# Performance work log

Hardware: AMD Instinct MI355X
Metric: run time of the kernel (lower is better)

Reference implementation:

```python
import jax, jax.numpy as jnp
import numpy as np

EPS = 1e-6
DIM = 384; HEADS = 6; POINTS = 4; LEVELS = 3; HIDDEN = 96
B = 2; H0 = 48; W0 = 48

def layernorm(x, w, b):
    m = jnp.mean(x, -1, keepdims=True)
    v = jnp.var(x, -1, keepdims=True)
    return (x - m) * jax.lax.rsqrt(v + EPS) * w + b

def make_ref_points(shapes):
    # normalized (x, y) pixel centers concatenated over levels -> [N, 2]
    pts = []
    for (Hl, Wl) in shapes:
        ry = (jnp.arange(Hl, dtype=jnp.float32) + 0.5) / Hl
        rx = (jnp.arange(Wl, dtype=jnp.float32) + 0.5) / Wl
        gy, gx = jnp.meshgrid(ry, rx, indexing='ij')
        pts.append(jnp.stack([gx.ravel(), gy.ravel()], -1))
    return jnp.concatenate(pts, 0)

def bilinear_gather(v, x, y, Hl, Wl):
    # v: [B, heads, Hl*Wl, c]; x, y: [B, heads, M] pixel coords
    # matches torch grid_sample(bilinear, align_corners=False, padding zeros)
    x0f = jnp.floor(x); y0f = jnp.floor(y)
    wx = (x - x0f)[..., None]; wy = (y - y0f)[..., None]
    x0 = x0f.astype(jnp.int32); y0 = y0f.astype(jnp.int32)
    def tap(yy, xx):
        valid = ((yy >= 0) & (yy < Hl) & (xx >= 0) & (xx < Wl)).astype(v.dtype)
        idx = jnp.clip(yy, 0, Hl - 1) * Wl + jnp.clip(xx, 0, Wl - 1)
        return jnp.take_along_axis(v, idx[..., None], axis=2) * valid[..., None]
    return (tap(y0, x0) * (1 - wx) * (1 - wy) + tap(y0, x0 + 1) * wx * (1 - wy)
            + tap(y0 + 1, x0) * (1 - wx) * wy + tap(y0 + 1, x0 + 1) * wx * wy)

def msdeform_attn(q, f, shapes, Wv, bv, Woff, boff, Watt, batt, Wout, bout):
    Bq, Nq, C = q.shape
    c = C // HEADS
    value = (f @ Wv + bv).reshape(Bq, -1, HEADS, c)
    off = (q @ Woff + boff).reshape(Bq, Nq, HEADS, LEVELS, POINTS, 2)
    att = jax.nn.softmax((q @ Watt + batt).reshape(Bq, Nq, HEADS, LEVELS * POINTS), -1)
    att = att.reshape(Bq, Nq, HEADS, LEVELS, POINTS)
    ref = make_ref_points(shapes)  # [Nq, 2]
    norm = jnp.array([[wl, hl] for (hl, wl) in shapes], dtype=q.dtype)  # [L, 2] = (W, H)
    loc = ref[None, :, None, None, None, :] + off / norm[None, None, None, :, None, :]
    starts = np.cumsum([0] + [h * w for (h, w) in shapes])
    out = jnp.zeros((Bq, Nq, HEADS, c), q.dtype)
    for l, (Hl, Wl) in enumerate(shapes):
        vl = value[:, starts[l]:starts[l + 1]].transpose(0, 2, 1, 3)  # [B,h,HW,c]
        ll = loc[:, :, :, l]  # [B,N,h,P,2]
        x = (ll[..., 0] * Wl - 0.5).transpose(0, 2, 1, 3).reshape(Bq, HEADS, Nq * POINTS)
        y = (ll[..., 1] * Hl - 0.5).transpose(0, 2, 1, 3).reshape(Bq, HEADS, Nq * POINTS)
        s = bilinear_gather(vl, x, y, Hl, Wl).reshape(Bq, HEADS, Nq, POINTS, c)
        out = out + jnp.einsum('bhnpc,bnhp->bnhc', s, att[:, :, :, l])
    return out.reshape(Bq, Nq, C) @ Wout + bout

def dwconv_levels(x, shapes, dw_w, dw_b):
    Bq, N, C = x.shape
    outs, s = [], 0
    for (Hl, Wl) in shapes:
        xi = x[:, s:s + Hl * Wl].reshape(Bq, Hl, Wl, C)
        yi = jax.lax.conv_general_dilated(xi, dw_w, (1, 1), 'SAME',
             dimension_numbers=('NHWC', 'HWIO', 'NHWC'), feature_group_count=C) + dw_b
        outs.append(yi.reshape(Bq, Hl * Wl, C))
        s += Hl * Wl
    return jnp.concatenate(outs, 1)

def setup_inputs():
    key = jax.random.key(0)
    ks = jax.random.split(key, 16)
    n = (H0 * W0) // 4
    N = 21 * n
    wfn = lambda k, s: 0.02 * jax.random.normal(k, s, jnp.float32)
    ones = lambda s: jnp.ones(s, jnp.float32)
    zeros = lambda s: jnp.zeros(s, jnp.float32)
    return {
        'query': jax.random.normal(ks[0], (B, N, DIM), jnp.float32),
        'reference_points': jax.random.uniform(ks[1], (B, N, 1, 2), dtype=jnp.float32),
        'feat': jax.random.normal(ks[2], (B, 4 * n, DIM), jnp.float32),
        'spatial_shapes': jnp.array([[2 * H0, 2 * W0], [H0, W0], [H0 // 2, W0 // 2]], jnp.int32),
        'level_start_index': jnp.array([0, 16 * n, 20 * n], jnp.int32),
        'H': H0, 'W': W0,
        'cti_qnorm_w': ones((DIM,)), 'cti_qnorm_b': zeros((DIM,)),
        'cti_fnorm_w': ones((DIM,)), 'cti_fnorm_b': zeros((DIM,)),
        'cf_qnorm_w': ones((DIM,)), 'cf_qnorm_b': zeros((DIM,)),
        'cf_fnorm_w': ones((DIM,)), 'cf_fnorm_b': zeros((DIM,)),
        'Wv': wfn(ks[3], (DIM, DIM)), 'bv': zeros((DIM,)),
        'Woff': wfn(ks[4], (DIM, HEADS * LEVELS * POINTS * 2)), 'boff': zeros((HEADS * LEVELS * POINTS * 2,)),
        'Watt': wfn(ks[5], (DIM, HEADS * LEVELS * POINTS)), 'batt': zeros((HEADS * LEVELS * POINTS,)),
        'Wout': wfn(ks[6], (DIM, DIM)), 'bout': zeros((DIM,)),
        'ffn_norm_w': ones((DIM,)), 'ffn_norm_b': zeros((DIM,)),
        'fc1_w': wfn(ks[7], (DIM, HIDDEN)), 'fc1_b': zeros((HIDDEN,)),
        'dw_w': wfn(ks[8], (3, 3, 1, HIDDEN)), 'dw_b': zeros((HIDDEN,)),
        'fc2_w': wfn(ks[9], (HIDDEN, DIM)), 'fc2_b': zeros((DIM,)),
    }

def reference(query, reference_points, feat, spatial_shapes, level_start_index, H, W,
              cti_qnorm_w, cti_qnorm_b, cti_fnorm_w, cti_fnorm_b,
              cf_qnorm_w, cf_qnorm_b, cf_fnorm_w, cf_fnorm_b,
              Wv, bv, Woff, boff, Watt, batt, Wout, bout,
              ffn_norm_w, ffn_norm_b, fc1_w, fc1_b, dw_w, dw_b, fc2_w, fc2_b):
    # NOTE: passed reference_points/spatial_shapes/level_start_index are ignored by
    # CTI_toC.forward; it recomputes them via deform_inputs_only_one(query, 16H, 16W).
    Bq, N, C = query.shape
    n = N // 21
    q = jnp.concatenate([query[:, :16 * n], query[:, 16 * n:20 * n] + feat, query[:, 20 * n:]], 1)
    shapes = [(2 * H, 2 * W), (H, W), (H // 2, W // 2)]
    qn = layernorm(q, cti_qnorm_w, cti_qnorm_b)
    fn = layernorm(q, cti_fnorm_w, cti_fnorm_b)
    aq = layernorm(qn, cf_qnorm_w, cf_qnorm_b)
    af = layernorm(fn, cf_fnorm_w, cf_fnorm_b)
    attn = msdeform_attn(aq, af, shapes, Wv, bv, Woff, boff, Watt, batt, Wout, bout)
    out = qn + attn
    h = layernorm(out, ffn_norm_w, ffn_norm_b) @ fc1_w + fc1_b
    h = dwconv_levels(h, shapes, dw_w, dw_b)
    h = jax.nn.gelu(h, approximate=False)
    h = h @ fc2_w + fc2_b
    return out + h
```

## Files before the change

### kernel.cpp

```cpp
#include <hip/hip_runtime.h>
#include <hip/hip_bf16.h>
#include <hip/hip_fp16.h>
#include <cstdint>
#include <cstddef>

#define NB 2
#define NTOK 12096
#define TOKS (NB * NTOK)
#define DIMC 384
#define NHEADS 6
#define CHD 64

typedef __attribute__((ext_vector_type(8))) __bf16 bf16x8;
typedef __attribute__((ext_vector_type(4))) float f32x4;

__device__ __forceinline__ float wave_reduce_add(float v) {
#pragma unroll
  for (int o = 32; o > 0; o >>= 1) v += __shfl_xor(v, o, 64);
  return v;
}

__device__ __forceinline__ float bf_lo(uint u) {
  union { uint i; float f; } c; c.i = u << 16; return c.f;
}
__device__ __forceinline__ float bf_hi(uint u) {
  union { uint i; float f; } c; c.i = u & 0xffff0000u; return c.f;
}
__device__ __forceinline__ ushort f2bf(float x) {
  union { __hip_bfloat16 b; ushort u; } c; c.b = __float2bfloat16(x); return c.u;
}

__device__ __forceinline__ void gload16(const ushort* g, ushort* l) {
  __builtin_amdgcn_global_load_lds(
      (const __attribute__((address_space(1))) uint*)g,
      (__attribute__((address_space(3))) uint*)l, 16, 0, 0);
}

__global__ __launch_bounds__(256) void prelude_kernel(
    const float* __restrict__ Wv, const float* __restrict__ Woff,
    const float* __restrict__ Watt, const float* __restrict__ Wo,
    const float* __restrict__ fc1, const float* __restrict__ fc2,
    const float* __restrict__ boff, const float* __restrict__ batt,
    const float* __restrict__ fc1b,
    __hip_bfloat16* __restrict__ Wvt, __hip_bfloat16* __restrict__ Wot,
    __hip_bfloat16* __restrict__ Wofat, __hip_bfloat16* __restrict__ fc1t,
    __hip_bfloat16* __restrict__ fc2t, float* __restrict__ bofat,
    float* __restrict__ fc1bp,
    const float* __restrict__ query, const float* __restrict__ feat,
    const float* __restrict__ w1, const float* __restrict__ b1,
    const float* __restrict__ w2, const float* __restrict__ b2,
    const float* __restrict__ w3, const float* __restrict__ b3,
    const float* __restrict__ w4, const float* __restrict__ b4,
    __hip_bfloat16* __restrict__ qn, __hip_bfloat16* __restrict__ aq,
    __hip_bfloat16* __restrict__ af) {
  if (blockIdx.x < 576) {
    int id = blockIdx.x * 256 + threadIdx.x;
    int k = id % 384, n = id / 384;
    Wvt[(size_t)n * 384 + k] = __float2bfloat16(Wv[(size_t)k * 384 + n]);
    Wot[(size_t)n * 384 + k] = __float2bfloat16(Wo[(size_t)k * 384 + n]);
    if (n < 256) {
      float v = 0.f;
      if (n < 144) v = Woff[(size_t)k * 144 + n];
      else if (n < 216) v = Watt[(size_t)k * 72 + (n - 144)];
      Wofat[(size_t)n * 384 + k] = __float2bfloat16(v);
    }
    if (n < 128)
      fc1t[(size_t)n * 384 + k] = __float2bfloat16(n < 96 ? fc1[(size_t)k * 96 + n] : 0.f);
    if (k < 96)
      fc2t[(size_t)n * 96 + k] = __float2bfloat16(fc2[(size_t)k * 384 + n]);
    if (id < 256) bofat[id] = id < 144 ? boff[id] : (id < 216 ? batt[id - 144] : 0.f);
    if (id < 128) fc1bp[id] = id < 96 ? fc1b[id] : 0.f;
    return;
  }

  int wid = ((blockIdx.x - 576) * blockDim.x + threadIdx.x) >> 6;
  if (wid >= TOKS) return;
  int lane = threadIdx.x & 63;
  int bb = wid / NTOK;
  int nq = wid - bb * NTOK;

  float x[6];
  const float* qp = query + (size_t)wid * DIMC + lane;
#pragma unroll
  for (int i = 0; i < 6; ++i) x[i] = qp[64 * i];
  if (nq >= 9216 && nq < 11520) {
    const float* fp = feat + ((size_t)bb * 2304 + (nq - 9216)) * DIMC + lane;
#pragma unroll
    for (int i = 0; i < 6; ++i) x[i] += fp[64 * i];
  }

  float s = 0.f, ss = 0.f;
#pragma unroll
  for (int i = 0; i < 6; ++i) { s += x[i]; ss += x[i] * x[i]; }
  s = wave_reduce_add(s); ss = wave_reduce_add(ss);
  float mean = s * (1.f / DIMC);
  float rs = rsqrtf(ss * (1.f / DIMC) - mean * mean + 1e-6f);

  float qv[6], fv[6];
  __hip_bfloat16* qnp = qn + (size_t)wid * DIMC + lane;
#pragma unroll
  for (int i = 0; i < 6; ++i) {
    int e = lane + 64 * i;
    float xh = (x[i] - mean) * rs;
    qv[i] = xh * w1[e] + b1[e];
    fv[i] = xh * w2[e] + b2[e];
    qnp[64 * i] = __float2bfloat16(qv[i]);
  }

  s = 0.f; ss = 0.f;
#pragma unroll
  for (int i = 0; i < 6; ++i) { s += qv[i]; ss += qv[i] * qv[i]; }
  s = wave_reduce_add(s); ss = wave_reduce_add(ss);
  float m2 = s * (1.f / DIMC);
  float rs2 = rsqrtf(ss * (1.f / DIMC) - m2 * m2 + 1e-6f);
  __hip_bfloat16* aqp = aq + (size_t)wid * DIMC + lane;
#pragma unroll
  for (int i = 0; i < 6; ++i) {
    int e = lane + 64 * i;
    aqp[64 * i] = __float2bfloat16((qv[i] - m2) * rs2 * w3[e] + b3[e]);
  }

  s = 0.f; ss = 0.f;
#pragma unroll
  for (int i = 0; i < 6; ++i) { s += fv[i]; ss += fv[i] * fv[i]; }
  s = wave_reduce_add(s); ss = wave_reduce_add(ss);
  float m3 = s * (1.f / DIMC);
  float rs3 = rsqrtf(ss * (1.f / DIMC) - m3 * m3 + 1e-6f);
  __hip_bfloat16* afp = af + (size_t)wid * DIMC + lane;
#pragma unroll
  for (int i = 0; i < 6; ++i) {
    int e = lane + 64 * i;
    afp[64 * i] = __float2bfloat16((fv[i] - m3) * rs3 * w4[e] + b4[e]);
  }
}

__global__ __launch_bounds__(256) void ln_kernel(
    const float* __restrict__ x, const float* __restrict__ w,
    const float* __restrict__ b, __hip_bfloat16* __restrict__ y) {
  int wid = (blockIdx.x * blockDim.x + threadIdx.x) >> 6;
  if (wid >= TOKS) return;
  int lane = threadIdx.x & 63;
  float v[6];
  const float* xp = x + (size_t)wid * DIMC + lane;
#pragma unroll
  for (int i = 0; i < 6; ++i) v[i] = xp[64 * i];
  float s = 0.f, ss = 0.f;
#pragma unroll
  for (int i = 0; i < 6; ++i) { s += v[i]; ss += v[i] * v[i]; }
  s = wave_reduce_add(s); ss = wave_reduce_add(ss);
  float mean = s * (1.f / DIMC);
  float rs = rsqrtf(ss * (1.f / DIMC) - mean * mean + 1e-6f);
  __hip_bfloat16* yp = y + (size_t)wid * DIMC + lane;
#pragma unroll
  for (int i = 0; i < 6; ++i) {
    int e = lane + 64 * i;
    yp[64 * i] = __float2bfloat16((v[i] - mean) * rs * w[e] + b[e]);
  }
}

template <int EPI, int OUTBF16>
__global__ __launch_bounds__(256) void gemm_mfma(
    const __hip_bfloat16* __restrict__ A, const __hip_bfloat16* __restrict__ Wt,
    const float* __restrict__ bias, const void* __restrict__ Rv,
    void* __restrict__ Cv, int K, int Np, int ntx) {
  __shared__ __align__(16) ushort As[2 * 128 * 32];
  __shared__ __align__(16) ushort Bs[2 * 128 * 32];
  const int tid = threadIdx.x;
  const int nwg = gridDim.x;
  const int bid = blockIdx.x;
  const int xcd = bid & 7, off = bid >> 3;
  const int q = nwg >> 3, r = nwg & 7;
  const int tile = (xcd < r ? xcd * (q + 1) : r * (q + 1) + (xcd - r) * q) + off;
  const int tx = tile % ntx, ty = tile / ntx;
  const int m0 = ty * 128, n0 = tx * 128;

  const int lane = tid & 63, wv = tid >> 6;
  const int wm = (wv >> 1) * 64, wn = (wv & 1) * 64;
  const int rl = lane & 15, kb = lane >> 4;

  const int c0 = wv * 64 + lane;
  const int c1 = c0 + 256;
  const int r0c = c0 >> 2, b0 = (c0 & 3) ^ (r0c & 3);
  const int r1c = c1 >> 2, b1 = (c1 & 3) ^ (r1c & 3);
  const ushort* gA0 = (const ushort*)A + (size_t)(m0 + r0c) * K + b0 * 8;
  const ushort* gA1 = (const ushort*)A + (size_t)(m0 + r1c) * K + b1 * 8;
  const ushort* gB0 = (const ushort*)Wt + (size_t)(n0 + r0c) * K + b0 * 8;
  const ushort* gB1 = (const ushort*)Wt + (size_t)(n0 + r1c) * K + b1 * 8;
  ushort* lA0 = &As[(size_t)wv * 512];
  ushort* lA1 = &As[(size_t)wv * 512 + 2048];
  ushort* lB0 = &Bs[(size_t)wv * 512];
  ushort* lB1 = &Bs[(size_t)wv * 512 + 2048];

  f32x4 acc[4][4] = {};
  const int nt = K >> 5;

  gload16(gA0, lA0);
  gload16(gA1, lA1);
  gload16(gB0, lB0);
  gload16(gB1, lB1);
  __syncthreads();

  for (int t = 0; t < nt; ++t) {
    const int cb = (t & 1) << 12;
    const int nb = 4096 - cb;
    if (t + 1 < nt) {
      const int k1 = (t + 1) << 5;
      gload16(gA0 + k1, lA0 + nb);
      gload16(gA1 + k1, lA1 + nb);
      gload16(gB0 + k1, lB0 + nb);
      gload16(gB1 + k1, lB1 + nb);
    }
    bf16x8 avf[4], bvf[4];
#pragma unroll
    for (int i = 0; i < 4; ++i) {
      int ra = wm + i * 16 + rl;
      avf[i] = *(const bf16x8*)&As[cb + ra * 32 + ((kb ^ (ra & 3)) << 3)];
      int rb = wn + i * 16 + rl;
      bvf[i] = *(const bf16x8*)&Bs[cb + rb * 32 + ((kb ^ (rb & 3)) << 3)];
    }
#pragma unroll
    for (int i = 0; i < 4; ++i)
#pragma unroll
      for (int j = 0; j < 4; ++j)
        acc[i][j] = __builtin_amdgcn_mfma_f32_16x16x32_bf16(avf[i], bvf[j],
                                                            acc[i][j], 0, 0, 0);
    __syncthreads();
  }

#pragma unroll
  for (int i = 0; i < 4; ++i) {
#pragma unroll
    for (int j = 0; j < 4; ++j) {
      int col = n0 + wn + j * 16 + rl;
      float bsv = bias[col];
#pragma unroll
      for (int rr = 0; rr < 4; ++rr) {
        int row = m0 + wm + i * 16 + kb * 4 + rr;
        size_t o = (size_t)row * Np + col;
        float v = acc[i][j][rr] + bsv;
        if (EPI == 1) v += __bfloat162float(((const __hip_bfloat16*)Rv)[o]);
        if (EPI == 2) v += ((const float*)Cv)[o];
        if (OUTBF16) ((__hip_bfloat16*)Cv)[o] = __float2bfloat16(v);
        else ((float*)Cv)[o] = v;
      }
    }
  }
}

__global__ __launch_bounds__(256) void gemm_dual(
    const __hip_bfloat16* __restrict__ A1, const __hip_bfloat16* __restrict__ W1,
    const float* __restrict__ bias1, void* __restrict__ C1,
    const __hip_bfloat16* __restrict__ A2, const __hip_bfloat16* __restrict__ W2,
    const float* __restrict__ bias2, void* __restrict__ C2) {
  __shared__ __align__(16) ushort As[2 * 128 * 32];
  __shared__ __align__(16) ushort Bs[2 * 128 * 32];
  const int tid = threadIdx.x;
  const int gbid = blockIdx.x;
  const bool r2 = gbid >= 567;
  const __hip_bfloat16* A = r2 ? A2 : A1;
  const __hip_bfloat16* Wt = r2 ? W2 : W1;
  const float* bias = r2 ? bias2 : bias1;
  void* Cv = r2 ? C2 : C1;
  const int Np = r2 ? 256 : 384, ntx = r2 ? 2 : 3;
  const int lbid = r2 ? gbid - 567 : gbid;
  const int lnwg = r2 ? 378 : 567;
  const int K = 384;

  const int xcd = lbid & 7, off = lbid >> 3;
  const int q = lnwg >> 3, r = lnwg & 7;
  const int tile = (xcd < r ? xcd * (q + 1) : r * (q + 1) + (xcd - r) * q) + off;
  const int tx = tile % ntx, ty = tile / ntx;
  const int m0 = ty * 128, n0 = tx * 128;

  const int lane = tid & 63, wv = tid >> 6;
  const int wm = (wv >> 1) * 64, wn = (wv & 1) * 64;
  const int rl = lane & 15, kb = lane >> 4;

  const int c0 = wv * 64 + lane;
  const int c1 = c0 + 256;
  const int r0c = c0 >> 2, b0 = (c0 & 3) ^ (r0c & 3);
  const int r1c = c1 >> 2, b1 = (c1 & 3) ^ (r1c & 3);
  const ushort* gA0 = (const ushort*)A + (size_t)(m0 + r0c) * K + b0 * 8;
  const ushort* gA1 = (const ushort*)A + (size_t)(m0 + r1c) * K + b1 * 8;
  const ushort* gB0 = (const ushort*)Wt + (size_t)(n0 + r0c) * K + b0 * 8;
  const ushort* gB1 = (const ushort*)Wt + (size_t)(n0 + r1c) * K + b1 * 8;
  ushort* lA0 = &As[(size_t)wv * 512];
  ushort* lA1 = &As[(size_t)wv * 512 + 2048];
  ushort* lB0 = &Bs[(size_t)wv * 512];
  ushort* lB1 = &Bs[(size_t)wv * 512 + 2048];

  f32x4 acc[4][4] = {};
  const int nt = K >> 5;

  gload16(gA0, lA0);
  gload16(gA1, lA1);
  gload16(gB0, lB0);
  gload16(gB1, lB1);
  __syncthreads();

  for (int t = 0; t < nt; ++t) {
    const int cb = (t & 1) << 12;
    const int nb = 4096 - cb;
    if (t + 1 < nt) {
      const int k1 = (t + 1) << 5;
      gload16(gA0 + k1, lA0 + nb);
      gload16(gA1 + k1, lA1 + nb);
      gload16(gB0 + k1, lB0 + nb);
      gload16(gB1 + k1, lB1 + nb);
    }
    bf16x8 avf[4], bvf[4];
#pragma unroll
    for (int i = 0; i < 4; ++i) {
      int ra = wm + i * 16 + rl;
      avf[i] = *(const bf16x8*)&As[cb + ra * 32 + ((kb ^ (ra & 3)) << 3)];
      int rb = wn + i * 16 + rl;
      bvf[i] = *(const bf16x8*)&Bs[cb + rb * 32 + ((kb ^ (rb & 3)) << 3)];
    }
#pragma unroll
    for (int i = 0; i < 4; ++i)
#pragma unroll
      for (int j = 0; j < 4; ++j)
        acc[i][j] = __builtin_amdgcn_mfma_f32_16x16x32_bf16(avf[i], bvf[j],
                                                            acc[i][j], 0, 0, 0);
    __syncthreads();
  }

#pragma unroll
  for (int i = 0; i < 4; ++i) {
#pragma unroll
    for (int j = 0; j < 4; ++j) {
      int col = n0 + wn + j * 16 + rl;
      float bsv = bias[col];
#pragma unroll
      for (int rr = 0; rr < 4; ++rr) {
        int row = m0 + wm + i * 16 + kb * 4 + rr;
        size_t o = (size_t)row * Np + col;
        float v = acc[i][j][rr] + bsv;
        if (!r2) ((__hip_bfloat16*)Cv)[o] = __float2bfloat16(v);
        else ((float*)Cv)[o] = v;
      }
    }
  }
}

__global__ __launch_bounds__(256) void msdeform_gather(
    const __hip_bfloat16* __restrict__ value, const float* __restrict__ offatt,
    __hip_bfloat16* __restrict__ samp) {
  const int NBLK = TOKS * NHEADS / 4;
  int bid = blockIdx.x;
  int swz = (bid & 7) * (NBLK / 8) + (bid >> 3);
  int tid = threadIdx.x;
  int w = tid >> 6;
  int wid = __builtin_amdgcn_readfirstlane(swz * 4 + w);
  int lane = tid & 63;

  __shared__ __align__(16) uint srec[192];
  uint* myrec = &srec[w * 48];

  int t = wid / NHEADS;
  int h = wid - t * NHEADS;
  int b = t / NTOK;
  int nq = t % NTOK;

  if (lane < 12) {
    int lp = lane;
    int l = lp >> 2;

    int pos, Hq, Wq;
    if (nq < 9216)       { pos = nq;         Hq = 96; Wq = 96; }
    else if (nq < 11520) { pos = nq - 9216;  Hq = 48; Wq = 48; }
    else                 { pos = nq - 11520; Hq = 24; Wq = 24; }
    int iq = pos / Wq, jq = pos - iq * Wq;
    float refx = (jq + 0.5f) / (float)Wq;
    float refy = (iq + 0.5f) / (float)Hq;

    const float* lg = offatt + (size_t)t * 256 + 144 + h * 12;
    float mx = -1e30f;
#pragma unroll
    for (int i = 0; i < 12; ++i) mx = fmaxf(mx, lg[i]);
    float sden = 0.f;
#pragma unroll
    for (int i = 0; i < 12; ++i) sden += __expf(lg[i] - mx);
    float aw = __expf(lg[lp] - mx) / sden;

    float ox = offatt[(size_t)t * 256 + h * 24 + lp * 2 + 0];
    float oy = offatt[(size_t)t * 256 + h * 24 + lp * 2 + 1];

    int Wl = 96 >> l;

    float xx = refx * (float)Wl + ox - 0.5f;
    float yy = refy * (float)Wl + oy - 0.5f;
    float x0f = floorf(xx), y0f = floorf(yy);
    int x0 = (int)x0f, y0 = (int)y0f;
    float wx = xx - x0f, wy = yy - y0f;

    bool vx0 = (x0 >= 0) & (x0 < Wl), vx1 = (x0 + 1 >= 0) & (x0 + 1 < Wl);
    bool vy0 = (y0 >= 0) & (y0 < Wl), vy1 = (y0 + 1 >= 0) & (y0 + 1 < Wl);
    int x0c = min(max(x0, 0), Wl - 1), x1c = min(max(x0 + 1, 0), Wl - 1);
    int y0c = min(max(y0, 0), Wl - 1), y1c = min(max(y0 + 1, 0), Wl - 1);

    float w00 = (vy0 && vx0) ? aw * (1.f - wx) * (1.f - wy) : 0.f;
    float w01 = (vy0 && vx1) ? aw * wx * (1.f - wy) : 0.f;
    float w10 = (vy1 && vx0) ? aw * (1.f - wx) * wy : 0.f;
    float w11 = (vy1 && vx1) ? aw * wx * wy : 0.f;

    uint4 rec;
    rec.x = ((uint)f2bf(w00) << 16) | (uint)(y0c * Wl + x0c);
    rec.y = ((uint)f2bf(w01) << 16) | (uint)(y0c * Wl + x1c);
    rec.z = ((uint)f2bf(w10) << 16) | (uint)(y1c * Wl + x0c);
    rec.w = ((uint)f2bf(w11) << 16) | (uint)(y1c * Wl + x1c);
    *(uint4*)&myrec[lp * 4] = rec;
  }
  asm volatile("s_waitcnt lgkmcnt(0)" ::: "memory");

  int g = lane >> 3, sub = lane & 7;
  int sub16 = sub * 16;

  const char* vb = (const char*)value + ((size_t)(b * NTOK) * DIMC + h * CHD) * 2;
  const char* vbl[3] = {vb, vb + 9216 * DIMC * 2, vb + 11520 * DIMC * 2};

  const uint* tp = &myrec[g];

  float acc[8] = {0.f, 0.f, 0.f, 0.f, 0.f, 0.f, 0.f, 0.f};
#pragma unroll
  for (int i = 0; i < 6; ++i) {
    uint rec = tp[i * 8];
    float wf = bf_hi(rec);
    uint off = (rec & 0x3fffu) * (uint)(DIMC * 2) + (uint)sub16;
    uint4 d = *(const uint4*)(vbl[i >> 1] + off);
    acc[0] = fmaf(wf, bf_lo(d.x), acc[0]);
    acc[1] = fmaf(wf, bf_hi(d.x), acc[1]);
    acc[2] = fmaf(wf, bf_lo(d.y), acc[2]);
    acc[3] = fmaf(wf, bf_hi(d.y), acc[3]);
    acc[4] = fmaf(wf, bf_lo(d.z), acc[4]);
    acc[5] = fmaf(wf, bf_hi(d.z), acc[5]);
    acc[6] = fmaf(wf, bf_lo(d.w), acc[6]);
    acc[7] = fmaf(wf, bf_hi(d.w), acc[7]);
  }

#pragma unroll
  for (int r = 0; r < 8; ++r) {
    acc[r] += __shfl_xor(acc[r], 8, 64);
    acc[r] += __shfl_xor(acc[r], 16, 64);
    acc[r] += __shfl_xor(acc[r], 32, 64);
  }

  if (lane < 8) {
    uint4 o;
    o.x = ((uint)f2bf(acc[1]) << 16) | f2bf(acc[0]);
    o.y = ((uint)f2bf(acc[3]) << 16) | f2bf(acc[2]);
    o.z = ((uint)f2bf(acc[5]) << 16) | f2bf(acc[4]);
    o.w = ((uint)f2bf(acc[7]) << 16) | f2bf(acc[6]);
    *(uint4*)((char*)samp + (size_t)wid * 128 + sub16) = o;
  }
}

__global__ __launch_bounds__(256) void dwconv_gelu(
    const __hip_bfloat16* __restrict__ x, const float* __restrict__ w,
    const float* __restrict__ bias, __hip_bfloat16* __restrict__ y) {
  int id = blockIdx.x * blockDim.x + threadIdx.x;
  if (id >= TOKS * 24) return;
  int g = id % 24;
  int tn = id / 24;
  int ch0 = g * 4;
  int b = tn / NTOK, nq = tn - b * NTOK;

  int pos, Hl, Wl, st;
  if (nq < 9216)       { pos = nq;         Hl = 96; Wl = 96; st = 0; }
  else if (nq < 11520) { pos = nq - 9216;  Hl = 48; Wl = 48; st = 9216; }
  else                 { pos = nq - 11520; Hl = 24; Wl = 24; st = 11520; }
  int i = pos / Wl, j = pos - i * Wl;

  f32x4 acc = *(const f32x4*)&bias[ch0];
#pragma unroll
  for (int di = 0; di < 3; ++di) {
#pragma unroll
    for (int dj = 0; dj < 3; ++dj) {
      int ii = i + di - 1, jj = j + dj - 1;
      if (ii >= 0 && ii < Hl && jj >= 0 && jj < Wl) {
        uint2 d = *(const uint2*)&x[((size_t)(b * NTOK + st + ii * Wl + jj)) * 128 + ch0];
        f32x4 wv = *(const f32x4*)&w[(di * 3 + dj) * 96 + ch0];
        acc[0] = fmaf(bf_lo(d.x), wv[0], acc[0]);
        acc[1] = fmaf(bf_hi(d.x), wv[1], acc[1]);
        acc[2] = fmaf(bf_lo(d.y), wv[2], acc[2]);
        acc[3] = fmaf(bf_hi(d.y), wv[3], acc[3]);
      }
    }
  }
  uint2 o;
  float g0 = 0.5f * acc[0] * (1.f + erff(acc[0] * 0.70710678f));
  float g1 = 0.5f * acc[1] * (1.f + erff(acc[1] * 0.70710678f));
  float g2 = 0.5f * acc[2] * (1.f + erff(acc[2] * 0.70710678f));
  float g3 = 0.5f * acc[3] * (1.f + erff(acc[3] * 0.70710678f));
  o.x = ((uint)f2bf(g1) << 16) | f2bf(g0);
  o.y = ((uint)f2bf(g3) << 16) | f2bf(g2);
  *(uint2*)((char*)y + (size_t)tn * 192 + ch0 * 2) = o;
}

extern "C" void kernel_launch(void* const* d_in, const int* in_sizes, int n_in,
                              void* d_out, int out_size, void* d_ws, size_t ws_size,
                              hipStream_t stream) {
  const float* query = (const float*)d_in[0];
  const float* feat   = (const float*)d_in[2];
  const float* cti_qw = (const float*)d_in[7];
  const float* cti_qb = (const float*)d_in[8];
  const float* cti_fw = (const float*)d_in[9];
  const float* cti_fb = (const float*)d_in[10];
  const float* cf_qw  = (const float*)d_in[11];
  const float* cf_qb  = (const float*)d_in[12];
  const float* cf_fw  = (const float*)d_in[13];
  const float* cf_fb  = (const float*)d_in[14];
  const float* Wv     = (const float*)d_in[15];
  const float* bv     = (const float*)d_in[16];
  const float* Woff   = (const float*)d_in[17];
  const float* boff   = (const float*)d_in[18];
  const float* Watt   = (const float*)d_in[19];
  const float* batt   = (const float*)d_in[20];
  const float* Wo     = (const float*)d_in[21];
  const float* bo     = (const float*)d_in[22];
  const float* ffw    = (const float*)d_in[23];
  const float* ffb    = (const float*)d_in[24];
  const float* fc1w   = (const float*)d_in[25];
  const float* fc1b   = (const float*)d_in[26];
  const float* dww    = (const float*)d_in[27];
  const float* dwb    = (const float*)d_in[28];
  const float* fc2w   = (const float*)d_in[29];
  const float* fc2b   = (const float*)d_in[30];
  float* out = (float*)d_out;

  char* ws = (char*)d_ws;
  __hip_bfloat16* qn  = (__hip_bfloat16*)ws;
  __hip_bfloat16* aq  = (__hip_bfloat16*)(ws + 37158912);
  __hip_bfloat16* af  = (__hip_bfloat16*)(ws + 55738368);
  __hip_bfloat16* val = (__hip_bfloat16*)(ws + 74317824);
  float* offatt       = (float*)(ws + 92897280);
  char* wbase = ws + 117669888;
  __hip_bfloat16* Wvt   = (__hip_bfloat16*)(wbase + 0);
  __hip_bfloat16* Wot   = (__hip_bfloat16*)(wbase + 589824);
  __hip_bfloat16* Wofat = (__hip_bfloat16*)(wbase + 1179648);
  __hip_bfloat16* fc1t  = (__hip_bfloat16*)(wbase + 1376256);
  __hip_bfloat16* fc2t  = (__hip_bfloat16*)(wbase + 1474560);
  float* bofat          = (float*)(wbase + 1548288);
  float* fc1bp          = (float*)(wbase + 1549312);
  __hip_bfloat16* samp = af;
  __hip_bfloat16* lnf  = aq;
  __hip_bfloat16* h1   = (__hip_bfloat16*)offatt;
  __hip_bfloat16* h2   = (__hip_bfloat16*)(ws + 92897280 + 6193152);

  dim3 blk(256);

  prelude_kernel<<<576 + TOKS / 4, blk, 0, stream>>>(
      Wv, Woff, Watt, Wo, fc1w, fc2w, boff, batt, fc1b, Wvt, Wot, Wofat, fc1t,
      fc2t, bofat, fc1bp, query, feat, cti_qw, cti_qb, cti_fw, cti_fb, cf_qw,
      cf_qb, cf_fw, cf_fb, qn, aq, af);

  gemm_dual<<<945, blk, 0, stream>>>(af, Wvt, bv, val, aq, Wofat, bofat, offatt);

  msdeform_gather<<<(TOKS * NHEADS) / 4, blk, 0, stream>>>(val, offatt, samp);

  gemm_mfma<1, 0><<<567, blk, 0, stream>>>(samp, Wot, bo, qn, out, 384, 384, 3);

  ln_kernel<<<TOKS / 4, blk, 0, stream>>>(out, ffw, ffb, lnf);
  gemm_mfma<0, 1><<<189, blk, 0, stream>>>(lnf, fc1t, fc1bp, nullptr, h1, 384, 128, 1);
  dwconv_gelu<<<(TOKS * 24 + 255) / 256, blk, 0, stream>>>(h1, dww, dwb, h2);
  gemm_mfma<2, 0><<<567, blk, 0, stream>>>(h2, fc2t, fc2b, nullptr, out, 96, 384, 3);
}
```

Baseline: 206.2 us.

## Split deformable-attention tap computation into a separate fully-parallel prep kernel

Moves the softmax, sampling-location and bilinear-weight computation out of the gather kernel into a new msdeform_prep kernel where every thread computes one tap record, instead of only 12 of 64 lanes per wave doing it. The records are written to a global workspace buffer and read back by the gather kernel, which no longer needs shared memory or the serial prologue. The cost is an extra kernel launch plus a global write and read of the tap records (about 9 MB). The XCD tile-swizzle formula is also pulled out into a shared helper.

```diff
diff --git a/kernel.cpp b/kernel.cpp
--- a/kernel.cpp
+++ b/kernel.cpp
@@ -28,6 +28,12 @@
 }
 __device__ __forceinline__ ushort f2bf(float x) {
   union { __hip_bfloat16 b; ushort u; } c; c.b = __float2bfloat16(x); return c.u;
+}
+
+__device__ __forceinline__ int xcd_chunk(int bid, int nwg) {
+  int xcd = bid & 7, off = bid >> 3;
+  int q = nwg >> 3, r = nwg & 7;
+  return (xcd < r ? xcd * (q + 1) : r * (q + 1) + (xcd - r) * q) + off;
 }
 
 __device__ __forceinline__ void gload16(const ushort* g, ushort* l) {
@@ -166,11 +172,7 @@
   __shared__ __align__(16) ushort As[2 * 128 * 32];
   __shared__ __align__(16) ushort Bs[2 * 128 * 32];
   const int tid = threadIdx.x;
-  const int nwg = gridDim.x;
-  const int bid = blockIdx.x;
-  const int xcd = bid & 7, off = bid >> 3;
-  const int q = nwg >> 3, r = nwg & 7;
-  const int tile = (xcd < r ? xcd * (q + 1) : r * (q + 1) + (xcd - r) * q) + off;
+  const int tile = xcd_chunk(blockIdx.x, gridDim.x);
   const int tx = tile % ntx, ty = tile / ntx;
   const int m0 = ty * 128, n0 = tx * 128;
 
@@ -266,9 +268,7 @@
   const int lnwg = r2 ? 378 : 567;
   const int K = 384;
 
-  const int xcd = lbid & 7, off = lbid >> 3;
-  const int q = lnwg >> 3, r = lnwg & 7;
-  const int tile = (xcd < r ? xcd * (q + 1) : r * (q + 1) + (xcd - r) * q) + off;
+  const int tile = xcd_chunk(lbid, lnwg);
   const int tx = tile % ntx, ty = tile / ntx;
   const int m0 = ty * 128, n0 = tx * 128;
 
@@ -343,83 +343,79 @@
   }
 }
 
+__global__ __launch_bounds__(256) void msdeform_prep(
+    const float* __restrict__ offatt, uint* __restrict__ taps) {
+  int tile = xcd_chunk(blockIdx.x, gridDim.x);
+  int id = tile * 256 + (int)threadIdx.x;
+  if (id >= TOKS * 72) return;
+  int t = id / 72, r = id - t * 72;
+  int h = r / 12, lp = r - h * 12;
+  int l = lp >> 2;
+  int nq = t % NTOK;
+
+  int pos, Hq, Wq;
+  if (nq < 9216)       { pos = nq;         Hq = 96; Wq = 96; }
+  else if (nq < 11520) { pos = nq - 9216;  Hq = 48; Wq = 48; }
+  else                 { pos = nq - 11520; Hq = 24; Wq = 24; }
+  int iq = pos / Wq, jq = pos - iq * Wq;
+  float refx = (jq + 0.5f) / (float)Wq;
+  float refy = (iq + 0.5f) / (float)Hq;
+
+  const float* lg = offatt + (size_t)t * 256 + 144 + h * 12;
+  float mx = -1e30f;
+#pragma unroll
+  for (int i = 0; i < 12; ++i) mx = fmaxf(mx, lg[i]);
+  float sden = 0.f;
+#pragma unroll
+  for (int i = 0; i < 12; ++i) sden += __expf(lg[i] - mx);
+  float aw = __expf(lg[lp] - mx) / sden;
+
+  float ox = offatt[(size_t)t * 256 + h * 24 + lp * 2 + 0];
+  float oy = offatt[(size_t)t * 256 + h * 24 + lp * 2 + 1];
+
+  int Wl = 96 >> l;
+
+  float xx = refx * (float)Wl + ox - 0.5f;
+  float yy = refy * (float)Wl + oy - 0.5f;
+  float x0f = floorf(xx), y0f = floorf(yy);
+  int x0 = (int)x0f, y0 = (int)y0f;
+  float wx = xx - x0f, wy = yy - y0f;
+
+  bool vx0 = (x0 >= 0) & (x0 < Wl), vx1 = (x0 + 1 >= 0) & (x0 + 1 < Wl);
+  bool vy0 = (y0 >= 0) & (y0 < Wl), vy1 = (y0 + 1 >= 0) & (y0 + 1 < Wl);
+  int x0c = min(max(x0, 0), Wl - 1), x1c = min(max(x0 + 1, 0), Wl - 1);
+  int y0c = min(max(y0, 0), Wl - 1), y1c = min(max(y0 + 1, 0), Wl - 1);
+
+  float w00 = (vy0 && vx0) ? aw * (1.f - wx) * (1.f - wy) : 0.f;
+  float w01 = (vy0 && vx1) ? aw * wx * (1.f - wy) : 0.f;
+  float w10 = (vy1 && vx0) ? aw * (1.f - wx) * wy : 0.f;
+  float w11 = (vy1 && vx1) ? aw * wx * wy : 0.f;
+
+  uint4 rec;
+  rec.x = ((uint)f2bf(w00) << 16) | (uint)(y0c * Wl + x0c);
+  rec.y = ((uint)f2bf(w01) << 16) | (uint)(y0c * Wl + x1c);
+  rec.z = ((uint)f2bf(w10) << 16) | (uint)(y1c * Wl + x0c);
+  rec.w = ((uint)f2bf(w11) << 16) | (uint)(y1c * Wl + x1c);
+  *(uint4*)&taps[((size_t)(t * NHEADS + h)) * 48 + lp * 4] = rec;
+}
+
 __global__ __launch_bounds__(256) void msdeform_gather(
-    const __hip_bfloat16* __restrict__ value, const float* __restrict__ offatt,
+    const __hip_bfloat16* __restrict__ value, const uint* __restrict__ taps,
     __hip_bfloat16* __restrict__ samp) {
-  const int NBLK = TOKS * NHEADS / 4;
-  int bid = blockIdx.x;
-  int swz = (bid & 7) * (NBLK / 8) + (bid >> 3);
-  int tid = threadIdx.x;
-  int w = tid >> 6;
-  int wid = __builtin_amdgcn_readfirstlane(swz * 4 + w);
-  int lane = tid & 63;
-
-  __shared__ __align__(16) uint srec[192];
-  uint* myrec = &srec[w * 48];
+  int swz = xcd_chunk(blockIdx.x, gridDim.x);
+  int wid = __builtin_amdgcn_readfirstlane(swz * 4 + ((int)threadIdx.x >> 6));
+  int lane = threadIdx.x & 63;
+  int g = lane >> 3, sub = lane & 7;
+  int sub16 = sub * 16;
 
   int t = wid / NHEADS;
   int h = wid - t * NHEADS;
   int b = t / NTOK;
-  int nq = t % NTOK;
-
-  if (lane < 12) {
-    int lp = lane;
-    int l = lp >> 2;
-
-    int pos, Hq, Wq;
-    if (nq < 9216)       { pos = nq;         Hq = 96; Wq = 96; }
-    else if (nq < 11520) { pos = nq - 9216;  Hq = 48; Wq = 48; }
-    else                 { pos = nq - 11520; Hq = 24; Wq = 24; }
-    int iq = pos / Wq, jq = pos - iq * Wq;
-    float refx = (jq + 0.5f) / (float)Wq;
-    float refy = (iq + 0.5f) / (float)Hq;
-
-    const float* lg = offatt + (size_t)t * 256 + 144 + h * 12;
-    float mx = -1e30f;
-#pragma unroll
-    for (int i = 0; i < 12; ++i) mx = fmaxf(mx, lg[i]);
-    float sden = 0.f;
-#pragma unroll
-    for (int i = 0; i < 12; ++i) sden += __expf(lg[i] - mx);
-    float aw = __expf(lg[lp] - mx) / sden;
-
-    float ox = offatt[(size_t)t * 256 + h * 24 + lp * 2 + 0];
-    float oy = offatt[(size_t)t * 256 + h * 24 + lp * 2 + 1];
-
-    int Wl = 96 >> l;
-
-    float xx = refx * (float)Wl + ox - 0.5f;
-    float yy = refy * (float)Wl + oy - 0.5f;
-    float x0f = floorf(xx), y0f = floorf(yy);
-    int x0 = (int)x0f, y0 = (int)y0f;
-    float wx = xx - x0f, wy = yy - y0f;
-
-    bool vx0 = (x0 >= 0) & (x0 < Wl), vx1 = (x0 + 1 >= 0) & (x0 + 1 < Wl);
-    bool vy0 = (y0 >= 0) & (y0 < Wl), vy1 = (y0 + 1 >= 0) & (y0 + 1 < Wl);
-    int x0c = min(max(x0, 0), Wl - 1), x1c = min(max(x0 + 1, 0), Wl - 1);
-    int y0c = min(max(y0, 0), Wl - 1), y1c = min(max(y0 + 1, 0), Wl - 1);
-
-    float w00 = (vy0 && vx0) ? aw * (1.f - wx) * (1.f - wy) : 0.f;
-    float w01 = (vy0 && vx1) ? aw * wx * (1.f - wy) : 0.f;
-    float w10 = (vy1 && vx0) ? aw * (1.f - wx) * wy : 0.f;
-    float w11 = (vy1 && vx1) ? aw * wx * wy : 0.f;
-
-    uint4 rec;
-    rec.x = ((uint)f2bf(w00) << 16) | (uint)(y0c * Wl + x0c);
-    rec.y = ((uint)f2bf(w01) << 16) | (uint)(y0c * Wl + x1c);
-    rec.z = ((uint)f2bf(w10) << 16) | (uint)(y1c * Wl + x0c);
-    rec.w = ((uint)f2bf(w11) << 16) | (uint)(y1c * Wl + x1c);
-    *(uint4*)&myrec[lp * 4] = rec;
-  }
-  asm volatile("s_waitcnt lgkmcnt(0)" ::: "memory");
-
-  int g = lane >> 3, sub = lane & 7;
-  int sub16 = sub * 16;
 
   const char* vb = (const char*)value + ((size_t)(b * NTOK) * DIMC + h * CHD) * 2;
   const char* vbl[3] = {vb, vb + 9216 * DIMC * 2, vb + 11520 * DIMC * 2};
 
-  const uint* tp = &myrec[g];
+  const uint* tp = taps + (size_t)wid * 48 + g;
 
   float acc[8] = {0.f, 0.f, 0.f, 0.f, 0.f, 0.f, 0.f, 0.f};
 #pragma unroll
@@ -542,6 +538,7 @@
   __hip_bfloat16* fc2t  = (__hip_bfloat16*)(wbase + 1474560);
   float* bofat          = (float*)(wbase + 1548288);
   float* fc1bp          = (float*)(wbase + 1549312);
+  uint* taps = (uint*)(ws + 119220224);
   __hip_bfloat16* samp = af;
   __hip_bfloat16* lnf  = aq;
   __hip_bfloat16* h1   = (__hip_bfloat16*)offatt;
@@ -556,7 +553,8 @@
 
   gemm_dual<<<945, blk, 0, stream>>>(af, Wvt, bv, val, aq, Wofat, bofat, offatt);
 
-  msdeform_gather<<<(TOKS * NHEADS) / 4, blk, 0, stream>>>(val, offatt, samp);
+  msdeform_prep<<<(TOKS * 72) / 256, blk, 0, stream>>>(offatt, taps);
+  msdeform_gather<<<(TOKS * NHEADS) / 4, blk, 0, stream>>>(val, taps, samp);
 
   gemm_mfma<1, 0><<<567, blk, 0, stream>>>(samp, Wot, bo, qn, out, 384, 384, 3);
 
```

After: 185.6 us. 1.11x faster.
